# Optimization experiments

Measured on AMD Instinct MI355X. Metric: run time of the kernel, lower is better.

## Reference

```python
import jax, jax.numpy as jnp
from jax import lax
import numpy as np

B, H, W, C = 512, 64, 128, 3
FEAT = 13 * 26 * 64  # ceil(64/5)*ceil(128/5)*(32+32) after SAME stride-5 convs + concat


def setup_inputs() -> dict:
    key = jax.random.key(0)
    ks = jax.random.split(key, 6)
    x = jax.random.normal(ks[0], (B, H, W, C), jnp.float32)
    conv0_w = jax.random.normal(ks[1], (3, 3, 3, 32), jnp.float32) * 0.05  # HWIO
    conv1_w = jax.random.normal(ks[2], (5, 5, 3, 32), jnp.float32) * 0.05
    fc0_w = jax.random.normal(ks[3], (FEAT, 32), jnp.float32) * 0.01
    fc0_b = jnp.zeros((32,), jnp.float32)
    fc1_w = jax.random.normal(ks[4], (32, 6), jnp.float32) * 0.1
    fc1_b = jnp.zeros((6,), jnp.float32)
    return {"x": x, "conv0_w": conv0_w, "conv1_w": conv1_w,
            "fc0_w": fc0_w, "fc0_b": fc0_b, "fc1_w": fc1_w, "fc1_b": fc1_b}


def _stn_forward(x, conv0_w, conv1_w, fc0_w, fc0_b, fc1_w, fc1_b):
    b, h, w, c = x.shape
    dn = ("NHWC", "HWIO", "NHWC")
    # ---- LocNet ----
    # AveragePooling2D(3x3, stride 1, SAME); TF avg_pool averages over valid
    # (non-padded) elements only, so normalize by a window-count map.
    psum = lax.reduce_window(x, 0.0, lax.add, (1, 3, 3, 1), (1, 1, 1, 1), "SAME")
    cnt = lax.reduce_window(jnp.ones((1, h, w, 1), x.dtype), 0.0, lax.add,
                            (1, 3, 3, 1), (1, 1, 1, 1), "SAME")
    pooled = psum / cnt
    x0 = jax.nn.relu(lax.conv_general_dilated(pooled, conv0_w, (5, 5), "SAME",
                                              dimension_numbers=dn))
    x1 = jax.nn.relu(lax.conv_general_dilated(x, conv1_w, (5, 5), "SAME",
                                              dimension_numbers=dn))
    feat = jnp.concatenate([x0, x1], axis=-1).reshape(b, -1)
    # Dropout(0.5) is identity at inference.
    hid = jnp.tanh(feat @ fc0_w + fc0_b)
    theta = jnp.tanh(hid @ fc1_w + fc1_b).reshape(b, 2, 3)
    # ---- gen_grid ----
    xt, yt = jnp.meshgrid(jnp.linspace(-1.0, 1.0, w), jnp.linspace(-1.0, 1.0, h))
    grid = jnp.stack([xt.ravel(), yt.ravel(), jnp.ones(h * w, x.dtype)])  # [3, h*w]
    T = jnp.einsum("bij,jk->bik", theta, grid)          # [b, 2, h*w]
    T = T.reshape(b, 2, h, w).transpose(0, 2, 3, 1)     # [b, h, w, 2]
    # ---- grid_sample (bilinear) ----
    gx = (T[..., 0] + 1.0) * w / 2.0
    gy = (T[..., 1] + 1.0) * h / 2.0
    x0f = jnp.clip(jnp.floor(gx), 0.0, w - 2.0)
    x1f = jnp.clip(jnp.floor(gx) + 1.0, 1.0, w - 1.0)
    y0f = jnp.clip(jnp.floor(gy), 0.0, h - 2.0)
    y1f = jnp.clip(jnp.floor(gy) + 1.0, 1.0, h - 1.0)
    xi0, xi1 = x0f.astype(jnp.int32), x1f.astype(jnp.int32)
    yi0, yi1 = y0f.astype(jnp.int32), y1f.astype(jnp.int32)
    bi = jnp.arange(b)[:, None, None]                   # broadcast batch index
    Q00 = x[bi, yi0, xi0]  # [b, h, w, c]
    Q01 = x[bi, yi1, xi0]
    Q10 = x[bi, yi0, xi1]
    Q11 = x[bi, yi1, xi1]
    wx0 = (x1f - gx)[..., None]
    wx1 = (gx - x0f)[..., None]
    wy0 = (y1f - gy)[..., None]
    wy1 = (gy - y0f)[..., None]
    # Wx @ Q @ Wy expanded: rows of Q are x-neighbors, cols are y-neighbors.
    out = wx0 * (wy0 * Q00 + wy1 * Q01) + wx1 * (wy0 * Q10 + wy1 * Q11)
    Wd = ((x1f - x0f) * (y1f - y0f))[..., None]
    return out / Wd


def reference(x, conv0_w, conv1_w, fc0_w, fc0_b, fc1_w, fc1_b):
    return _stn_forward(x, conv0_w, conv1_w, fc0_w, fc0_b, fc1_w, fc1_b)
```

## Files before the change

### kernel.cpp

```cpp
#include <hip/hip_runtime.h>
#include <math.h>

namespace {
constexpr int BN = 512, HH = 64, WW = 128, CC = 3;
constexpr int OHH = 13, OWW = 26;
constexpr int NPOS = OHH * OWW;
constexpr int NSLAB = NPOS * 2;
constexpr int PCH = 26;
constexpr int NPC = NSLAB / PCH;
}

__global__ __launch_bounds__(256) void k_locnet(const float* __restrict__ x,
                                                const float* __restrict__ w0,
                                                const float* __restrict__ w1,
                                                const float* __restrict__ fw0,
                                                float* __restrict__ part) {
  const int cpx = (NPOS * 4) >> 3;
  const int L = (blockIdx.x & 7) * cpx + (blockIdx.x >> 3);
  const int bc = L / NPOS;
  const int pos = L - bc * NPOS;
  const int oh = pos / OWW, ow = pos - oh * OWW;
  const int role = threadIdx.x >> 7;
  const int b = bc * 128 + (threadIdx.x & 127);
  const float* xb = x + (size_t)b * (HH * WW * CC);

  const int rbase = oh * 5 - 1 + role;
  float xv[5][15];
  if (ow > 0 && ow < OWW - 1) {
    float4 q[5][4];
#pragma unroll
    for (int ri = 0; ri < 5; ++ri) {
      const int gr = rbase + ri;
      if (gr >= 0 && gr < HH) {
        const float* rp = xb + (size_t)gr * (WW * CC) + (ow * 5 - 1) * 3;
        q[ri][0] = *(const float4*)(rp);
        q[ri][1] = *(const float4*)(rp + 4);
        q[ri][2] = *(const float4*)(rp + 8);
        q[ri][3] = *(const float4*)(rp + 12);
      }
    }
#pragma unroll
    for (int ri = 0; ri < 5; ++ri) {
      const int gr = rbase + ri;
      if (gr < 0 || gr >= HH) {
#pragma unroll
        for (int c = 0; c < 15; ++c) xv[ri][c] = 0.f;
      } else {
        xv[ri][0] = q[ri][0].x; xv[ri][1] = q[ri][0].y; xv[ri][2] = q[ri][0].z;
        xv[ri][3] = q[ri][0].w; xv[ri][4] = q[ri][1].x; xv[ri][5] = q[ri][1].y;
        xv[ri][6] = q[ri][1].z; xv[ri][7] = q[ri][1].w; xv[ri][8] = q[ri][2].x;
        xv[ri][9] = q[ri][2].y; xv[ri][10] = q[ri][2].z; xv[ri][11] = q[ri][2].w;
        xv[ri][12] = q[ri][3].x; xv[ri][13] = q[ri][3].y; xv[ri][14] = q[ri][3].z;
      }
    }
  } else {
#pragma unroll
    for (int ri = 0; ri < 5; ++ri) {
      const int gr = rbase + ri;
      const int grc = min(max(gr, 0), HH - 1);
      const bool rv = (gr >= 0) & (gr < HH);
      const float* rowp = xb + grc * (WW * CC);
#pragma unroll
      for (int c = 0; c < 5; ++c) {
        const int gc = ow * 5 - 1 + c;
        const int gcc = min(max(gc, 0), WW - 1);
        const bool v = rv & (gc >= 0) & (gc < WW);
        const float* pp = rowp + gcc * CC;
        const float f0 = pp[0], f1 = pp[1], f2 = pp[2];
        xv[ri][c * 3 + 0] = v ? f0 : 0.f;
        xv[ri][c * 3 + 1] = v ? f1 : 0.f;
        xv[ri][c * 3 + 2] = v ? f2 : 0.f;
      }
    }
  }

  float hacc[32];
#pragma unroll
  for (int n = 0; n < 32; ++n) hacc[n] = 0.f;

  if (role == 0) {
    float pooled[27];
#pragma unroll
    for (int kh = 0; kh < 3; ++kh)
#pragma unroll
      for (int kw = 0; kw < 3; ++kw) {
        const int gr = oh * 5 + kh, gc = ow * 5 + kw;
        const int rc = min(gr + 1, HH - 1) - max(gr - 1, 0) + 1;
        const int c2 = min(gc + 1, WW - 1) - max(gc - 1, 0) + 1;
        const float inv = 1.0f / (float)(rc * c2);
#pragma unroll
        for (int ic = 0; ic < 3; ++ic) {
          float s = 0.f;
#pragma unroll
          for (int dr = 0; dr < 3; ++dr)
#pragma unroll
            for (int dc = 0; dc < 3; ++dc)
              s += xv[kh + dr][(kw + dc) * 3 + ic];
          pooled[(kh * 3 + kw) * 3 + ic] = s * inv;
        }
      }
#pragma unroll 1
    for (int qg = 0; qg < 8; ++qg) {
      float a0 = 0.f, a1 = 0.f, a2 = 0.f, a3 = 0.f;
#pragma unroll
      for (int tap = 0; tap < 27; ++tap) {
        const float pv = pooled[tap];
        const float4 wv = *(const float4*)(w0 + tap * 32 + qg * 4);
        a0 += pv * wv.x; a1 += pv * wv.y; a2 += pv * wv.z; a3 += pv * wv.w;
      }
      const float a[4] = {fmaxf(a0, 0.f), fmaxf(a1, 0.f),
                          fmaxf(a2, 0.f), fmaxf(a3, 0.f)};
      const float* wr = fw0 + ((size_t)pos * 64 + qg * 4) * 32;
#pragma unroll
      for (int j = 0; j < 4; ++j) {
        const float aj = a[j];
#pragma unroll
        for (int q2 = 0; q2 < 8; ++q2) {
          const float4 wv = *(const float4*)(wr + j * 32 + q2 * 4);
          hacc[q2 * 4 + 0] += aj * wv.x; hacc[q2 * 4 + 1] += aj * wv.y;
          hacc[q2 * 4 + 2] += aj * wv.z; hacc[q2 * 4 + 3] += aj * wv.w;
        }
      }
    }
  } else {
#pragma unroll 1
    for (int qg = 0; qg < 8; ++qg) {
      float a0 = 0.f, a1 = 0.f, a2 = 0.f, a3 = 0.f;
#pragma unroll
      for (int kh = 0; kh < 5; ++kh)
#pragma unroll
        for (int kw = 0; kw < 5; ++kw)
#pragma unroll
          for (int ic = 0; ic < 3; ++ic) {
            const float pv = xv[kh][kw * 3 + ic];
            const int tap = (kh * 5 + kw) * 3 + ic;
            const float4 wv = *(const float4*)(w1 + tap * 32 + qg * 4);
            a0 += pv * wv.x; a1 += pv * wv.y; a2 += pv * wv.z; a3 += pv * wv.w;
          }
      const float a[4] = {fmaxf(a0, 0.f), fmaxf(a1, 0.f),
                          fmaxf(a2, 0.f), fmaxf(a3, 0.f)};
      const float* wr = fw0 + ((size_t)pos * 64 + 32 + qg * 4) * 32;
#pragma unroll
      for (int j = 0; j < 4; ++j) {
        const float aj = a[j];
#pragma unroll
        for (int q2 = 0; q2 < 8; ++q2) {
          const float4 wv = *(const float4*)(wr + j * 32 + q2 * 4);
          hacc[q2 * 4 + 0] += aj * wv.x; hacc[q2 * 4 + 1] += aj * wv.y;
          hacc[q2 * 4 + 2] += aj * wv.z; hacc[q2 * 4 + 3] += aj * wv.w;
        }
      }
    }
  }

  float* po = part + (size_t)(pos * 2 + role) * 32 * 512 + b;
#pragma unroll
  for (int n = 0; n < 32; ++n) po[(size_t)n * 512] = hacc[n];
}

__global__ __launch_bounds__(256) void k_theta1(const float* __restrict__ part,
                                                float* __restrict__ part2) {
  const int pc = blockIdx.x >> 3;
  const int bcs = blockIdx.x & 7;
  const int lane = threadIdx.x & 63;
  const int og = threadIdx.x >> 6;
  const int bcol = bcs * 64 + lane;
  float acc[8] = {0.f, 0.f, 0.f, 0.f, 0.f, 0.f, 0.f, 0.f};
  const float* pp = part + ((size_t)pc * PCH * 32 + og * 8) * 512 + bcol;
  for (int pq = 0; pq < PCH; ++pq) {
#pragma unroll
    for (int j = 0; j < 8; ++j)
      acc[j] += pp[((size_t)pq * 32 + j) * 512];
  }
  float* o = part2 + ((size_t)pc * 32 + og * 8) * 512 + bcol;
#pragma unroll
  for (int j = 0; j < 8; ++j) o[(size_t)j * 512] = acc[j];
}

__global__ __launch_bounds__(256) void k_theta2(const float* __restrict__ part2,
                                                const float* __restrict__ b0,
                                                const float* __restrict__ w1f,
                                                const float* __restrict__ b1,
                                                float* __restrict__ theta) {
  __shared__ float hid[64][32];
  const int lane = threadIdx.x & 63;
  const int og = threadIdx.x >> 6;
  const int bcol = blockIdx.x * 64 + lane;
#pragma unroll
  for (int j = 0; j < 8; ++j) {
    const int oc = og * 8 + j;
    float s = b0[oc];
#pragma unroll
    for (int pc = 0; pc < NPC; ++pc)
      s += part2[((size_t)pc * 32 + oc) * 512 + bcol];
    hid[lane][oc] = tanhf(s);
  }
  __syncthreads();
  for (int u = threadIdx.x; u < 64 * 6; u += 256) {
    const int bl = u / 6, j = u - bl * 6;
    float s2 = b1[j];
#pragma unroll
    for (int oc = 0; oc < 32; ++oc) s2 += hid[bl][oc] * w1f[oc * 6 + j];
    theta[(blockIdx.x * 64 + bl) * 6 + j] = tanhf(s2);
  }
}

__global__ __launch_bounds__(256) void k_sample(const float* __restrict__ x,
                                                const float* __restrict__ theta,
                                                float* __restrict__ out) {
  const int b = blockIdx.x >> 3;
  const int seg = blockIdx.x & 7;
  __shared__ float th[6];
  if (threadIdx.x < 6) th[threadIdx.x] = theta[b * 6 + threadIdx.x];
  __syncthreads();
  const float t00 = th[0], t01 = th[1], t02 = th[2];
  const float t10 = th[3], t11 = th[4], t12 = th[5];
  const int idx = seg * 1024 + threadIdx.x * 4;
  const int i = idx >> 7, j0 = idx & 127;
  const float yt = (float)i * (2.0f / 63.0f) - 1.0f;
  const float* xb = x + (size_t)b * (HH * WW * CC);
  float res[12];
#pragma unroll
  for (int p = 0; p < 4; ++p) {
    const float xt = (float)(j0 + p) * (2.0f / 127.0f) - 1.0f;
    const float gx = (t00 * xt + t01 * yt + t02 + 1.0f) * 64.0f;
    const float gy = (t10 * xt + t11 * yt + t12 + 1.0f) * 32.0f;
    const float fx = floorf(gx), fy = floorf(gy);
    const float x0f = fminf(fmaxf(fx, 0.f), 126.f);
    const float x1f = fminf(fmaxf(fx + 1.f, 1.f), 127.f);
    const float y0f = fminf(fmaxf(fy, 0.f), 62.f);
    const float y1f = fminf(fmaxf(fy + 1.f, 1.f), 63.f);
    const float wx0 = x1f - gx, wx1 = gx - x0f;
    const float wy0 = y1f - gy, wy1 = gy - y0f;
    const int xi0 = (int)x0f, xi1 = (int)x1f;
    const int yi0 = (int)y0f, yi1 = (int)y1f;
    const float* q00 = xb + (yi0 * WW + xi0) * 3;
    const float* q01 = xb + (yi1 * WW + xi0) * 3;
    const float* q10 = xb + (yi0 * WW + xi1) * 3;
    const float* q11 = xb + (yi1 * WW + xi1) * 3;
#pragma unroll
    for (int c = 0; c < 3; ++c)
      res[p * 3 + c] = wx0 * (wy0 * q00[c] + wy1 * q01[c]) +
                       wx1 * (wy0 * q10[c] + wy1 * q11[c]);
  }
  float4* o = (float4*)(out + ((size_t)b * 8192 + idx) * 3);
  o[0] = make_float4(res[0], res[1], res[2], res[3]);
  o[1] = make_float4(res[4], res[5], res[6], res[7]);
  o[2] = make_float4(res[8], res[9], res[10], res[11]);
}

extern "C" void kernel_launch(void* const* d_in, const int* in_sizes, int n_in,
                              void* d_out, int out_size, void* d_ws, size_t ws_size,
                              hipStream_t stream) {
  (void)in_sizes; (void)n_in; (void)out_size; (void)ws_size;
  const float* x   = (const float*)d_in[0];
  const float* w0  = (const float*)d_in[1];
  const float* w1  = (const float*)d_in[2];
  const float* fw0 = (const float*)d_in[3];
  const float* fb0 = (const float*)d_in[4];
  const float* fw1 = (const float*)d_in[5];
  const float* fb1 = (const float*)d_in[6];
  float* outp = (float*)d_out;
  float* part  = outp;
  float* part2 = outp + (size_t)NSLAB * 32 * 512;
  float* theta = (float*)d_ws;
  k_locnet<<<NPOS * 4, 256, 0, stream>>>(x, w0, w1, fw0, part);
  k_theta1<<<NPC * 8, 256, 0, stream>>>(part, part2);
  k_theta2<<<8, 256, 0, stream>>>(part2, fb0, fw1, fb1, theta);
  k_sample<<<BN * 8, 256, 0, stream>>>(x, theta, outp);
}
```

Baseline: 136.8 us.

## Split locnet conv channels across waves with LDS-staged patches and in-block reduction

Reworks the locnet kernel so each block handles 64 batch items at one output position. The 6x15 input patches are staged through shared memory, and each of the four waves computes 8 channels of both convolutions instead of one conv branch per half-block. Partial FC0 sums are reduced across waves in LDS before a single write per position, which halves the partial buffer that k_theta1 must read. This brings more blocks, an LDS staging pass with extra syncs, a 90-float register array per thread, and duplicated pooling work in every wave.

```diff
diff --git a/kernel.cpp b/kernel.cpp
--- a/kernel.cpp
+++ b/kernel.cpp
@@ -5,157 +5,140 @@
 constexpr int BN = 512, HH = 64, WW = 128, CC = 3;
 constexpr int OHH = 13, OWW = 26;
 constexpr int NPOS = OHH * OWW;
-constexpr int NSLAB = NPOS * 2;
 constexpr int PCH = 26;
-constexpr int NPC = NSLAB / PCH;
-}
-
-__global__ __launch_bounds__(256) void k_locnet(const float* __restrict__ x,
-                                                const float* __restrict__ w0,
-                                                const float* __restrict__ w1,
-                                                const float* __restrict__ fw0,
-                                                float* __restrict__ part) {
-  const int cpx = (NPOS * 4) >> 3;
-  const int L = (blockIdx.x & 7) * cpx + (blockIdx.x >> 3);
+constexpr int NPC = NPOS / PCH;
+}
+
+__global__ __launch_bounds__(256, 3) void k_locnet(const float* __restrict__ x,
+                                                   const float* __restrict__ w0,
+                                                   const float* __restrict__ w1,
+                                                   const float* __restrict__ fw0,
+                                                   float* __restrict__ part) {
+  __shared__ float lds[6400];
+  const int L = (blockIdx.x & 7) * (NPOS * 8 / 8) + (blockIdx.x >> 3);
   const int bc = L / NPOS;
   const int pos = L - bc * NPOS;
   const int oh = pos / OWW, ow = pos - oh * OWW;
-  const int role = threadIdx.x >> 7;
-  const int b = bc * 128 + (threadIdx.x & 127);
-  const float* xb = x + (size_t)b * (HH * WW * CC);
-
-  const int rbase = oh * 5 - 1 + role;
-  float xv[5][15];
-  if (ow > 0 && ow < OWW - 1) {
-    float4 q[5][4];
-#pragma unroll
-    for (int ri = 0; ri < 5; ++ri) {
-      const int gr = rbase + ri;
-      if (gr >= 0 && gr < HH) {
-        const float* rp = xb + (size_t)gr * (WW * CC) + (ow * 5 - 1) * 3;
-        q[ri][0] = *(const float4*)(rp);
-        q[ri][1] = *(const float4*)(rp + 4);
-        q[ri][2] = *(const float4*)(rp + 8);
-        q[ri][3] = *(const float4*)(rp + 12);
+  const int b0 = bc * 64;
+
+  for (int k = 0; k < 24; ++k) {
+    const int f = threadIdx.x + (k << 8);
+    const int bi = f / 96;
+    const int r = f - bi * 96;
+    const int ri = r >> 4, s = r & 15;
+    if (s < 15) {
+      const int j = s / 3, ic = s - j * 3;
+      const int gr = oh * 5 - 1 + ri;
+      const int gc = ow * 5 - 1 + j;
+      float v = 0.f;
+      if (gr >= 0 && gr < HH && gc >= 0 && gc < WW)
+        v = x[(size_t)(b0 + bi) * (HH * WW * CC) + gr * (WW * CC) + gc * CC + ic];
+      lds[bi * 91 + ri * 15 + s] = v;
+    }
+  }
+  __syncthreads();
+
+  const int wv = __builtin_amdgcn_readfirstlane(threadIdx.x >> 6);
+  const int bl = threadIdx.x & 63;
+  float xr[90];
+  {
+    const int xbase = bl * 91;
+#pragma unroll
+    for (int t2 = 0; t2 < 90; ++t2) xr[t2] = lds[xbase + t2];
+  }
+
+  float hacc[32];
+#pragma unroll
+  for (int n = 0; n < 32; ++n) hacc[n] = 0.f;
+
+  float pooled[27];
+#pragma unroll
+  for (int kh = 0; kh < 3; ++kh)
+#pragma unroll
+    for (int kw = 0; kw < 3; ++kw) {
+      const int gr = oh * 5 + kh, gc = ow * 5 + kw;
+      const int rc = min(gr + 1, HH - 1) - max(gr - 1, 0) + 1;
+      const int c2 = min(gc + 1, WW - 1) - max(gc - 1, 0) + 1;
+      const float inv = 1.0f / (float)(rc * c2);
+#pragma unroll
+      for (int ic = 0; ic < 3; ++ic) {
+        float s = 0.f;
+#pragma unroll
+        for (int dr = 0; dr < 3; ++dr)
+#pragma unroll
+          for (int dc = 0; dc < 3; ++dc)
+            s += xr[(kh + dr) * 15 + (kw + dc) * 3 + ic];
+        pooled[(kh * 3 + kw) * 3 + ic] = s * inv;
       }
     }
-#pragma unroll
-    for (int ri = 0; ri < 5; ++ri) {
-      const int gr = rbase + ri;
-      if (gr < 0 || gr >= HH) {
-#pragma unroll
-        for (int c = 0; c < 15; ++c) xv[ri][c] = 0.f;
-      } else {
-        xv[ri][0] = q[ri][0].x; xv[ri][1] = q[ri][0].y; xv[ri][2] = q[ri][0].z;
-        xv[ri][3] = q[ri][0].w; xv[ri][4] = q[ri][1].x; xv[ri][5] = q[ri][1].y;
-        xv[ri][6] = q[ri][1].z; xv[ri][7] = q[ri][1].w; xv[ri][8] = q[ri][2].x;
-        xv[ri][9] = q[ri][2].y; xv[ri][10] = q[ri][2].z; xv[ri][11] = q[ri][2].w;
-        xv[ri][12] = q[ri][3].x; xv[ri][13] = q[ri][3].y; xv[ri][14] = q[ri][3].z;
+
+  {
+    float a[8] = {0.f, 0.f, 0.f, 0.f, 0.f, 0.f, 0.f, 0.f};
+#pragma unroll
+    for (int tap = 0; tap < 27; ++tap) {
+      const float pv = pooled[tap];
+      const float4 wa = *(const float4*)(w0 + tap * 32 + wv * 8);
+      const float4 wb = *(const float4*)(w0 + tap * 32 + wv * 8 + 4);
+      a[0] += pv * wa.x; a[1] += pv * wa.y; a[2] += pv * wa.z; a[3] += pv * wa.w;
+      a[4] += pv * wb.x; a[5] += pv * wb.y; a[6] += pv * wb.z; a[7] += pv * wb.w;
+    }
+#pragma unroll
+    for (int j = 0; j < 8; ++j) {
+      const float aj = fmaxf(a[j], 0.f);
+      const float* wr = fw0 + (size_t)(pos * 64 + wv * 8 + j) * 32;
+#pragma unroll
+      for (int q = 0; q < 8; ++q) {
+        const float4 w4 = *(const float4*)(wr + q * 4);
+        hacc[q * 4 + 0] += aj * w4.x; hacc[q * 4 + 1] += aj * w4.y;
+        hacc[q * 4 + 2] += aj * w4.z; hacc[q * 4 + 3] += aj * w4.w;
       }
     }
-  } else {
-#pragma unroll
-    for (int ri = 0; ri < 5; ++ri) {
-      const int gr = rbase + ri;
-      const int grc = min(max(gr, 0), HH - 1);
-      const bool rv = (gr >= 0) & (gr < HH);
-      const float* rowp = xb + grc * (WW * CC);
-#pragma unroll
-      for (int c = 0; c < 5; ++c) {
-        const int gc = ow * 5 - 1 + c;
-        const int gcc = min(max(gc, 0), WW - 1);
-        const bool v = rv & (gc >= 0) & (gc < WW);
-        const float* pp = rowp + gcc * CC;
-        const float f0 = pp[0], f1 = pp[1], f2 = pp[2];
-        xv[ri][c * 3 + 0] = v ? f0 : 0.f;
-        xv[ri][c * 3 + 1] = v ? f1 : 0.f;
-        xv[ri][c * 3 + 2] = v ? f2 : 0.f;
+  }
+
+  {
+    float a[8] = {0.f, 0.f, 0.f, 0.f, 0.f, 0.f, 0.f, 0.f};
+#pragma unroll
+    for (int kh = 0; kh < 5; ++kh)
+#pragma unroll
+      for (int kw = 0; kw < 5; ++kw)
+#pragma unroll
+        for (int ic = 0; ic < 3; ++ic) {
+          const float pv = xr[(kh + 1) * 15 + kw * 3 + ic];
+          const int tap = (kh * 5 + kw) * 3 + ic;
+          const float4 wa = *(const float4*)(w1 + tap * 32 + wv * 8);
+          const float4 wb = *(const float4*)(w1 + tap * 32 + wv * 8 + 4);
+          a[0] += pv * wa.x; a[1] += pv * wa.y; a[2] += pv * wa.z; a[3] += pv * wa.w;
+          a[4] += pv * wb.x; a[5] += pv * wb.y; a[6] += pv * wb.z; a[7] += pv * wb.w;
+        }
+#pragma unroll
+    for (int j = 0; j < 8; ++j) {
+      const float aj = fmaxf(a[j], 0.f);
+      const float* wr = fw0 + (size_t)(pos * 64 + 32 + wv * 8 + j) * 32;
+#pragma unroll
+      for (int q = 0; q < 8; ++q) {
+        const float4 w4 = *(const float4*)(wr + q * 4);
+        hacc[q * 4 + 0] += aj * w4.x; hacc[q * 4 + 1] += aj * w4.y;
+        hacc[q * 4 + 2] += aj * w4.z; hacc[q * 4 + 3] += aj * w4.w;
       }
     }
   }
 
-  float hacc[32];
-#pragma unroll
-  for (int n = 0; n < 32; ++n) hacc[n] = 0.f;
-
-  if (role == 0) {
-    float pooled[27];
-#pragma unroll
-    for (int kh = 0; kh < 3; ++kh)
-#pragma unroll
-      for (int kw = 0; kw < 3; ++kw) {
-        const int gr = oh * 5 + kh, gc = ow * 5 + kw;
-        const int rc = min(gr + 1, HH - 1) - max(gr - 1, 0) + 1;
-        const int c2 = min(gc + 1, WW - 1) - max(gc - 1, 0) + 1;
-        const float inv = 1.0f / (float)(rc * c2);
-#pragma unroll
-        for (int ic = 0; ic < 3; ++ic) {
-          float s = 0.f;
-#pragma unroll
-          for (int dr = 0; dr < 3; ++dr)
-#pragma unroll
-            for (int dc = 0; dc < 3; ++dc)
-              s += xv[kh + dr][(kw + dc) * 3 + ic];
-          pooled[(kh * 3 + kw) * 3 + ic] = s * inv;
-        }
-      }
-#pragma unroll 1
-    for (int qg = 0; qg < 8; ++qg) {
-      float a0 = 0.f, a1 = 0.f, a2 = 0.f, a3 = 0.f;
-#pragma unroll
-      for (int tap = 0; tap < 27; ++tap) {
-        const float pv = pooled[tap];
-        const float4 wv = *(const float4*)(w0 + tap * 32 + qg * 4);
-        a0 += pv * wv.x; a1 += pv * wv.y; a2 += pv * wv.z; a3 += pv * wv.w;
-      }
-      const float a[4] = {fmaxf(a0, 0.f), fmaxf(a1, 0.f),
-                          fmaxf(a2, 0.f), fmaxf(a3, 0.f)};
-      const float* wr = fw0 + ((size_t)pos * 64 + qg * 4) * 32;
-#pragma unroll
-      for (int j = 0; j < 4; ++j) {
-        const float aj = a[j];
-#pragma unroll
-        for (int q2 = 0; q2 < 8; ++q2) {
-          const float4 wv = *(const float4*)(wr + j * 32 + q2 * 4);
-          hacc[q2 * 4 + 0] += aj * wv.x; hacc[q2 * 4 + 1] += aj * wv.y;
-          hacc[q2 * 4 + 2] += aj * wv.z; hacc[q2 * 4 + 3] += aj * wv.w;
-        }
-      }
-    }
-  } else {
-#pragma unroll 1
-    for (int qg = 0; qg < 8; ++qg) {
-      float a0 = 0.f, a1 = 0.f, a2 = 0.f, a3 = 0.f;
-#pragma unroll
-      for (int kh = 0; kh < 5; ++kh)
-#pragma unroll
-        for (int kw = 0; kw < 5; ++kw)
-#pragma unroll
-          for (int ic = 0; ic < 3; ++ic) {
-            const float pv = xv[kh][kw * 3 + ic];
-            const int tap = (kh * 5 + kw) * 3 + ic;
-            const float4 wv = *(const float4*)(w1 + tap * 32 + qg * 4);
-            a0 += pv * wv.x; a1 += pv * wv.y; a2 += pv * wv.z; a3 += pv * wv.w;
-          }
-      const float a[4] = {fmaxf(a0, 0.f), fmaxf(a1, 0.f),
-                          fmaxf(a2, 0.f), fmaxf(a3, 0.f)};
-      const float* wr = fw0 + ((size_t)pos * 64 + 32 + qg * 4) * 32;
-#pragma unroll
-      for (int j = 0; j < 4; ++j) {
-        const float aj = a[j];
-#pragma unroll
-        for (int q2 = 0; q2 < 8; ++q2) {
-          const float4 wv = *(const float4*)(wr + j * 32 + q2 * 4);
-          hacc[q2 * 4 + 0] += aj * wv.x; hacc[q2 * 4 + 1] += aj * wv.y;
-          hacc[q2 * 4 + 2] += aj * wv.z; hacc[q2 * 4 + 3] += aj * wv.w;
-        }
-      }
-    }
-  }
-
-  float* po = part + (size_t)(pos * 2 + role) * 32 * 512 + b;
-#pragma unroll
-  for (int n = 0; n < 32; ++n) po[(size_t)n * 512] = hacc[n];
+  __syncthreads();
+  if (wv > 0) {
+    float* rp = &lds[(size_t)(wv - 1) * 64 * 33 + bl * 33];
+#pragma unroll
+    for (int n = 0; n < 32; ++n) rp[n] = hacc[n];
+  }
+  __syncthreads();
+  if (wv == 0) {
+    float* po = part + (size_t)pos * 32 * 512 + b0 + bl;
+#pragma unroll
+    for (int n = 0; n < 32; ++n) {
+      const float s = hacc[n] + lds[bl * 33 + n] + lds[64 * 33 + bl * 33 + n] +
+                      lds[128 * 33 + bl * 33 + n];
+      po[(size_t)n * 512] = s;
+    }
+  }
 }
 
 __global__ __launch_bounds__(256) void k_theta1(const float* __restrict__ part,
@@ -262,9 +245,9 @@
   const float* fb1 = (const float*)d_in[6];
   float* outp = (float*)d_out;
   float* part  = outp;
-  float* part2 = outp + (size_t)NSLAB * 32 * 512;
+  float* part2 = outp + (size_t)NPOS * 32 * 512;
   float* theta = (float*)d_ws;
-  k_locnet<<<NPOS * 4, 256, 0, stream>>>(x, w0, w1, fw0, part);
+  k_locnet<<<NPOS * 8, 256, 0, stream>>>(x, w0, w1, fw0, part);
   k_theta1<<<NPC * 8, 256, 0, stream>>>(part, part2);
   k_theta2<<<8, 256, 0, stream>>>(part2, fb0, fw1, fb1, theta);
   k_sample<<<BN * 8, 256, 0, stream>>>(x, theta, outp);
```

New measurement: 151.3 us. 1.11x slower.
